# Optimization experiments

Measured on AMD Instinct MI355X. Metric: run time of the kernel, lower is better.

## Reference

```python
import jax, jax.numpy as jnp
import numpy as np
from jax.scipy.special import logsumexp

B, T, H, L = 64, 512, 768, 9


def setup_inputs() -> dict:
    key = jax.random.key(0)
    ks = jax.random.split(key, 8)
    length = jax.random.randint(ks[0], (B,), 0, T, dtype=jnp.int32)
    word2vec = jax.random.normal(ks[1], (B, T, H), dtype=jnp.float32)
    mask = jnp.ones((B, T), dtype=jnp.int32)
    label = jax.random.randint(ks[2], (B, T), 0, L, dtype=jnp.int32)
    # Linear(768 -> num_labels) params (PyTorch default init scale)
    bound = 1.0 / np.sqrt(H)
    W = jax.random.uniform(ks[3], (L, H), jnp.float32, -bound, bound)
    b = jax.random.uniform(ks[4], (L,), jnp.float32, -bound, bound)
    # CRF params (torchcrf init: uniform(-0.1, 0.1))
    start_transitions = jax.random.uniform(ks[5], (L,), jnp.float32, -0.1, 0.1)
    end_transitions = jax.random.uniform(ks[6], (L,), jnp.float32, -0.1, 0.1)
    transitions = jax.random.uniform(ks[7], (L, L), jnp.float32, -0.1, 0.1)
    return {"length": length, "word2vec": word2vec, "mask": mask, "label": label,
            "W": W, "b": b, "start_transitions": start_transitions,
            "end_transitions": end_transitions, "transitions": transitions}


def _crf_nll(emissions, tags, mask, start_transitions, end_transitions, transitions):
    # emissions [B,T,L], tags [B,T] int, mask [B,T] {0,1}
    Bn, Tn, Ln = emissions.shape
    maskf = mask.astype(emissions.dtype)
    # ---- numerator: score of the given tag sequence ----
    batch = jnp.arange(Bn)
    score = start_transitions[tags[:, 0]] + emissions[batch, 0, tags[:, 0]]
    # transition scores for steps 1..T-1, vectorized over time
    trans_sc = transitions[tags[:, :-1], tags[:, 1:]]                    # [B,T-1]
    emit_sc = jnp.take_along_axis(emissions, tags[..., None], axis=2)[..., 0]  # [B,T]
    score = score + jnp.sum((trans_sc + emit_sc[:, 1:]) * maskf[:, 1:], axis=1)
    seq_ends = jnp.sum(mask, axis=1).astype(jnp.int32) - 1
    last_tags = tags[batch, seq_ends]
    numerator = score + end_transitions[last_tags]
    # ---- denominator: log partition via forward algorithm (scan over time) ----
    em_t = jnp.transpose(emissions, (1, 0, 2))   # [T,B,L]
    mk_t = jnp.transpose(mask, (1, 0)) != 0      # [T,B]
    alpha0 = start_transitions[None, :] + em_t[0]  # [B,L]

    def step(alpha, inp):
        em_i, m_i = inp
        # alpha[b, i] + transitions[i, j] + emissions[b, j]
        nxt = logsumexp(alpha[:, :, None] + transitions[None, :, :] + em_i[:, None, :], axis=1)
        alpha = jnp.where(m_i[:, None], nxt, alpha)
        return alpha, None

    alpha, _ = jax.lax.scan(step, alpha0, (em_t[1:], mk_t[1:]))
    denominator = logsumexp(alpha + end_transitions[None, :], axis=1)
    llh = numerator - denominator
    return -jnp.mean(llh)


def reference(length, word2vec, mask, label, W, b, start_transitions, end_transitions, transitions):
    # dropout p=0.0 -> identity; Linear projection to emissions
    emissions = jnp.einsum('bth,lh->btl', word2vec, W) + b  # [B,T,L]
    return _crf_nll(emissions, label, mask, start_transitions, end_transitions, transitions)
```

## Files before the change

### kernel.cpp

```cpp
#include <hip/hip_runtime.h>
#include <hip/hip_bf16.h>


#define Bn 64
#define Tn 512
#define Hn 768
#define Ln 9
#define EMS 12
#define CS 16
#define NCHO 4
#define OT 64
#define KSTEPS 24

typedef short bf16x8 __attribute__((ext_vector_type(8)));
typedef float f32x4  __attribute__((ext_vector_type(4)));

__device__ __forceinline__ short f2bf(float f) {
    return (short)__builtin_bit_cast(unsigned short, __float2bfloat16(f));
}

#define GLOAD16(gp, lp)                                                        \
    __builtin_amdgcn_global_load_lds(                                          \
        (const __attribute__((address_space(1))) void*)(gp),                   \
        (__attribute__((address_space(3))) void*)(lp), 16, 0, 0)

__device__ __forceinline__ void pair_combine(
    const float (*MA)[Ln], const float* lgA,
    const float (*MB)[Ln], const float* lgB,
    int r, float* outM, float* outLg)
{
    float mB = lgB[0];
#pragma unroll
    for (int k = 1; k < 9; ++k) mB = fmaxf(mB, lgB[k]);
    float tA[9];
#pragma unroll
    for (int k = 0; k < 9; ++k) tA[k] = MA[r][k] * __expf(lgB[k] - mB);
    float v[9];
#pragma unroll
    for (int jj = 0; jj < 9; ++jj) {
        float acc = tA[0] * MB[0][jj];
#pragma unroll
        for (int k = 1; k < 9; ++k) acc += tA[k] * MB[k][jj];
        v[jj] = acc;
    }
    float mx = v[0];
#pragma unroll
    for (int jj = 1; jj < 9; ++jj) mx = fmaxf(mx, v[jj]);
    float inv = 1.f / mx;
#pragma unroll
    for (int jj = 0; jj < 9; ++jj) outM[jj] = v[jj] * inv;
    *outLg = lgA[r] + mB + __logf(mx);
}

__global__ __launch_bounds__(256) void emis_o_kernel(
    const float* __restrict__ wv, const float* __restrict__ Wm,
    const float* __restrict__ bias, const int* __restrict__ mask,
    const int* __restrict__ label, const float* __restrict__ trans,
    const float* __restrict__ startT,
    float* __restrict__ Mq, float* __restrict__ lgq,
    float* __restrict__ numq, int* __restrict__ msq,
    float* __restrict__ em0, int* __restrict__ cnt)
{
    __shared__ bf16x8 wlds[KSTEPS * 64];
    __shared__ __align__(16) float bufA[4][3][512];
    __shared__ float ldsE[OT][EMS];
    __shared__ int   ldsM[OT];
    __shared__ float eTs[81];
    __shared__ float sM[NCHO][Ln][Ln];
    __shared__ float sLg[NCHO][Ln];
    __shared__ float s2M[2][Ln][Ln];
    __shared__ float s2Lg[2][Ln];

    const int tid   = threadIdx.x;
    const int lane  = tid & 63;
    const int wid   = tid >> 6;
    const int bid   = blockIdx.x;
    const int b     = bid >> 3;
    const int o     = bid & 7;
    const int tbase = o * OT;

    if (bid == 0 && tid == 0) cnt[0] = 0;
    if (tid < 81) eTs[tid] = __expf(trans[tid]);

    for (int idx = tid; idx < KSTEPS * 64; idx += 256) {
        const int kk = idx >> 6, ln = idx & 63;
        const int n = ln & 15, kb2 = ln >> 4;
        bf16x8 v;
        if (n < Ln) {
            const float* src = Wm + n * Hn + kk * 32 + kb2 * 8;
#pragma unroll
            for (int j = 0; j < 8; ++j) v[j] = f2bf(src[j]);
        } else {
#pragma unroll
            for (int j = 0; j < 8; ++j) v[j] = 0;
        }
        wlds[idx] = v;
    }
    __syncthreads();

    {
        const int rowbase = bid * OT + wid * 16;
        const int rr   = lane >> 3;
        const int colf = (((lane & 7) * 16) ^ (rr << 4)) >> 2;
        const float* g0 = wv + (size_t)(rowbase + rr) * Hn + colf;
        const float* g1 = g0 + 8 * Hn;
        float* lb = &bufA[wid][0][0];

        const int m  = lane & 15;
        const int kb = lane >> 4;
        const int ph0 = m * 32 + (((kb * 32)      ^ ((m & 7) << 4)) >> 2);
        const int ph1 = m * 32 + (((kb * 32 + 16) ^ ((m & 7) << 4)) >> 2);

        f32x4 acc = {0.f, 0.f, 0.f, 0.f};

        GLOAD16(g0,      lb);        GLOAD16(g1,      lb + 256);
        GLOAD16(g0 + 32, lb + 512);  GLOAD16(g1 + 32, lb + 768);

#define EMIS_STEP(KK, SLOT)                                                    \
        {                                                                      \
            const float* s_ = lb + (SLOT) * 512;                               \
            float4 x0 = *reinterpret_cast<const float4*>(s_ + ph0);            \
            float4 x1 = *reinterpret_cast<const float4*>(s_ + ph1);            \
            bf16x8 a;                                                          \
            a[0] = f2bf(x0.x); a[1] = f2bf(x0.y);                              \
            a[2] = f2bf(x0.z); a[3] = f2bf(x0.w);                              \
            a[4] = f2bf(x1.x); a[5] = f2bf(x1.y);                              \
            a[6] = f2bf(x1.z); a[7] = f2bf(x1.w);                              \
            bf16x8 bfr = wlds[(KK) * 64 + lane];                               \
            acc = __builtin_amdgcn_mfma_f32_16x16x32_bf16(a, bfr, acc, 0, 0, 0); \
        }

        for (int kk = 0; kk < KSTEPS - 2; ++kk) {
            const int sl2 = (kk + 2) % 3;
            GLOAD16(g0 + (kk + 2) * 32, lb + sl2 * 512);
            GLOAD16(g1 + (kk + 2) * 32, lb + sl2 * 512 + 256);
            asm volatile("s_waitcnt vmcnt(4)" ::: "memory");
            EMIS_STEP(kk, kk % 3);
        }
        asm volatile("s_waitcnt vmcnt(2)" ::: "memory");
        EMIS_STEP(KSTEPS - 2, (KSTEPS - 2) % 3);
        asm volatile("s_waitcnt vmcnt(0)" ::: "memory");
        EMIS_STEP(KSTEPS - 1, (KSTEPS - 1) % 3);
#undef EMIS_STEP

        const int l = lane & 15;
        if (l < Ln) {
            const float bl = bias[l];
#pragma unroll
            for (int r = 0; r < 4; ++r) {
                const int lrow = wid * 16 + (lane >> 4) * 4 + r;
                ldsE[lrow][l] = __expf(acc[r] + bl);
            }
        }
    }
    __syncthreads();

    if (wid == 0) {
        const int gt  = tbase + lane;
        const int tag = label[b * Tn + gt];
        const int mk  = mask[b * Tn + gt];
        ldsM[lane] = mk;
        float part = 0.f; int ms = mk;
        if (gt == 0) {
            part = startT[tag] + __logf(ldsE[0][tag]);
        } else if (mk) {
            const int prev = label[b * Tn + gt - 1];
            part = trans[prev * Ln + tag] + __logf(ldsE[lane][tag]);
        }
#pragma unroll
        for (int off = 32; off > 0; off >>= 1) {
            part += __shfl_xor(part, off);
            ms   += __shfl_xor(ms, off);
        }
        if (lane == 0) { numq[bid] = part; msq[bid] = ms; }
        if (o == 0 && lane < Ln) em0[b * Ln + lane] = ldsE[0][lane];

        if (tid < NCHO * Ln) {
            float Tr[81];
#pragma unroll
            for (int i = 0; i < 81; ++i) Tr[i] = eTs[i];
            const int r = tid % Ln;
            const int c = tid / Ln;

            float v[9];
#pragma unroll
            for (int k = 0; k < 9; ++k) v[k] = (k == r) ? 1.f : 0.f;
            float lg = 0.f;

            int t0 = tbase + c * CS; if (t0 == 0) t0 = 1;
            const int t1 = tbase + (c + 1) * CS;

            int lt = t0 - tbase;
            float4 e0v = *reinterpret_cast<const float4*>(&ldsE[lt][0]);
            float4 e1v = *reinterpret_cast<const float4*>(&ldsE[lt][4]);
            float  e8  = ldsE[lt][8];
            int    mk2 = ldsM[lt];

            for (int t = t0; t < t1; ++t) {
                float4 p0 = make_float4(0.f, 0.f, 0.f, 0.f), p1 = p0;
                float  p8 = 0.f; int pm = 0;
                if (t + 1 < t1) {
                    const int nlt = t + 1 - tbase;
                    p0 = *reinterpret_cast<const float4*>(&ldsE[nlt][0]);
                    p1 = *reinterpret_cast<const float4*>(&ldsE[nlt][4]);
                    p8 = ldsE[nlt][8];
                    pm = ldsM[nlt];
                }
                if (mk2) {
                    float e[9] = {e0v.x, e0v.y, e0v.z, e0v.w,
                                  e1v.x, e1v.y, e1v.z, e1v.w, e8};
                    float nv[9];
#pragma unroll
                    for (int jj = 0; jj < 9; ++jj) {
                        float acc = v[0] * Tr[jj];
#pragma unroll
                        for (int k = 1; k < 9; ++k) acc += v[k] * Tr[k * 9 + jj];
                        nv[jj] = acc * e[jj];
                    }
                    float mx = nv[0];
#pragma unroll
                    for (int jj = 1; jj < 9; ++jj) mx = fmaxf(mx, nv[jj]);
                    float inv = 1.f / mx;
#pragma unroll
                    for (int jj = 0; jj < 9; ++jj) v[jj] = nv[jj] * inv;
                    lg += __logf(mx);
                }
                e0v = p0; e1v = p1; e8 = p8; mk2 = pm;
            }
#pragma unroll
            for (int jj = 0; jj < 9; ++jj) sM[c][r][jj] = v[jj];
            sLg[c][r] = lg;
        }

        if (tid < 2 * Ln) {
            const int p = tid / Ln, r = tid % Ln;
            float om[9], ol;
            pair_combine(sM[2 * p], sLg[2 * p], sM[2 * p + 1], sLg[2 * p + 1],
                         r, om, &ol);
#pragma unroll
            for (int jj = 0; jj < 9; ++jj) s2M[p][r][jj] = om[jj];
            s2Lg[p][r] = ol;
        }

        if (tid < Ln) {
            const int r = tid;
            float om[9], ol;
            pair_combine(s2M[0], s2Lg[0], s2M[1], s2Lg[1], r, om, &ol);
#pragma unroll
            for (int jj = 0; jj < 9; ++jj) Mq[bid * 81 + r * 9 + jj] = om[jj];
            lgq[bid * Ln + r] = ol;
        }
    }
}

__global__ __launch_bounds__(64) void comb_kernel(
    const float* __restrict__ Mq, const float* __restrict__ lgq,
    const float* __restrict__ numq, const int* __restrict__ msq,
    const float* __restrict__ em0, const int* __restrict__ label,
    const float* __restrict__ startT, const float* __restrict__ endT,
    float* __restrict__ partial, int* __restrict__ cnt, float* __restrict__ out)
{
    __shared__ float cO[8][Ln][Ln];
    __shared__ float cOl[8][Ln];
    __shared__ float cQ[4][Ln][Ln];
    __shared__ float cQl[4][Ln];
    __shared__ float cem[Ln];
    __shared__ float cnum[8];
    __shared__ int   cms[8];

    const int b = blockIdx.x, tid = threadIdx.x;

    for (int i = tid; i < 8 * 81; i += 64) ((float*)cO)[i]  = Mq[b * 648 + i];
    for (int i = tid; i < 8 * 9;  i += 64) ((float*)cOl)[i] = lgq[b * 72 + i];
    if (tid < Ln) cem[tid] = em0[b * Ln + tid];
    if (tid < 8) { cnum[tid] = numq[b * 8 + tid]; cms[tid] = msq[b * 8 + tid]; }
    __syncthreads();

    if (tid < 4 * Ln) {
        const int p = tid / Ln, r = tid % Ln;
        float om[9], ol;
        pair_combine(cO[2 * p], cOl[2 * p], cO[2 * p + 1], cOl[2 * p + 1],
                     r, om, &ol);
#pragma unroll
        for (int jj = 0; jj < 9; ++jj) cQ[p][r][jj] = om[jj];
        cQl[p][r] = ol;
    }
    __syncthreads();

    if (tid < 16) {
        const int lj = tid;
        const float NEG = -1e30f;
        float la = (lj < Ln) ? (startT[lj] + __logf(cem[lj])) : NEG;
        for (int c = 0; c < 4; ++c) {
            float mc[9];
#pragma unroll
            for (int rr = 0; rr < 9; ++rr) mc[rr] = (lj < Ln) ? cQ[c][rr][lj] : 0.f;
            float x = (lj < Ln) ? (la + cQl[c][lj]) : NEG;
            float mm = x;
#pragma unroll
            for (int off = 1; off < 16; off <<= 1) mm = fmaxf(mm, __shfl_xor(mm, off, 16));
            float w = __expf(x - mm);
            float sacc = 0.f;
#pragma unroll
            for (int rr = 0; rr < 9; ++rr) sacc += __shfl(w, rr, 16) * mc[rr];
            la = (lj < Ln) ? (mm + __logf(sacc)) : NEG;
        }
        float x = (lj < Ln) ? (la + endT[lj]) : NEG;
        float mm = x;
#pragma unroll
        for (int off = 1; off < 16; off <<= 1) mm = fmaxf(mm, __shfl_xor(mm, off, 16));
        float se = __expf(x - mm);
#pragma unroll
        for (int off = 1; off < 16; off <<= 1) se += __shfl_xor(se, off, 16);
        if (lj == 0) {
            float denom = mm + __logf(se);
            float numer = cnum[0] + cnum[1] + cnum[2] + cnum[3]
                        + cnum[4] + cnum[5] + cnum[6] + cnum[7];
            int   sm    = cms[0] + cms[1] + cms[2] + cms[3]
                        + cms[4] + cms[5] + cms[6] + cms[7];
            int   last  = label[b * Tn + sm - 1];
            partial[b]  = denom - (numer + endT[last]);
        }
    }

    int old = 0;
    if (tid == 0) {
        __threadfence();
        old = atomicAdd(cnt, 1);
    }
    old = __shfl(old, 0);
    if (old == Bn - 1) {
        __threadfence();
        float pv = partial[tid];
#pragma unroll
        for (int off = 32; off > 0; off >>= 1) pv += __shfl_xor(pv, off);
        if (tid == 0) out[0] = pv * (1.0f / Bn);
    }
}

extern "C" void kernel_launch(void* const* d_in, const int* in_sizes, int n_in,
                              void* d_out, int out_size, void* d_ws, size_t ws_size,
                              hipStream_t stream)
{
    const float* wv    = (const float*)d_in[1];
    const int*   mask  = (const int*)d_in[2];
    const int*   label = (const int*)d_in[3];
    const float* Wm    = (const float*)d_in[4];
    const float* bias  = (const float*)d_in[5];
    const float* st    = (const float*)d_in[6];
    const float* en    = (const float*)d_in[7];
    const float* tr    = (const float*)d_in[8];

    float* ws      = (float*)d_ws;
    float* Mq      = ws;
    float* lgq     = ws + 41472;
    float* numq    = ws + 46080;
    int*   msq     = (int*)(ws + 46592);
    float* em0     = ws + 47104;
    float* partial = ws + 47680;
    int*   cnt     = (int*)(ws + 47744);
    float* out     = (float*)d_out;

    hipLaunchKernelGGL(emis_o_kernel, dim3(512), dim3(256), 0, stream,
                       wv, Wm, bias, mask, label, tr, st,
                       Mq, lgq, numq, msq, em0, cnt);
    hipLaunchKernelGGL(comb_kernel, dim3(Bn), dim3(64), 0, stream,
                       Mq, lgq, numq, msq, em0, label, st, en,
                       partial, cnt, out);
}
```

Baseline: 42.21 us.

## Replace MFMA emission GEMM with fp32 register dot products and per-wave scans

The bf16 MFMA projection is removed, along with its global_load_lds triple-buffered staging and the weight staging in LDS. In its place each lane keeps its slice of W in registers, does fp32 FMAs over direct float4 loads of word2vec, and reduces each row across the wave with shuffles. The numerator and CRF chunk scans are also spread across all four waves, each handling its own 16 rows, instead of running in wave 0 only, which removes one block-wide barrier. The cost is many cross-lane shuffles per row, heavy register use for W, and only shallow memory prefetching from the unroll-by-2 loop, in exchange for exact fp32 emissions.

Result: slower. 53.08 us (+25.8%).

```diff
diff --git a/kernel.cpp b/kernel.cpp
--- a/kernel.cpp
+++ b/kernel.cpp
@@ -1,5 +1,4 @@
 #include <hip/hip_runtime.h>
-#include <hip/hip_bf16.h>
 
 
 #define Bn 64
@@ -7,22 +6,8 @@
 #define Hn 768
 #define Ln 9
 #define EMS 12
-#define CS 16
+#define OT 64
 #define NCHO 4
-#define OT 64
-#define KSTEPS 24
-
-typedef short bf16x8 __attribute__((ext_vector_type(8)));
-typedef float f32x4  __attribute__((ext_vector_type(4)));
-
-__device__ __forceinline__ short f2bf(float f) {
-    return (short)__builtin_bit_cast(unsigned short, __float2bfloat16(f));
-}
-
-#define GLOAD16(gp, lp)                                                        \
-    __builtin_amdgcn_global_load_lds(                                          \
-        (const __attribute__((address_space(1))) void*)(gp),                   \
-        (__attribute__((address_space(3))) void*)(lp), 16, 0, 0)
 
 __device__ __forceinline__ void pair_combine(
     const float (*MA)[Ln], const float* lgA,
@@ -61,15 +46,14 @@
     float* __restrict__ numq, int* __restrict__ msq,
     float* __restrict__ em0, int* __restrict__ cnt)
 {
-    __shared__ bf16x8 wlds[KSTEPS * 64];
-    __shared__ __align__(16) float bufA[4][3][512];
-    __shared__ float ldsE[OT][EMS];
+    __shared__ __align__(16) float ldsE[OT][EMS];
     __shared__ int   ldsM[OT];
-    __shared__ float eTs[81];
     __shared__ float sM[NCHO][Ln][Ln];
     __shared__ float sLg[NCHO][Ln];
     __shared__ float s2M[2][Ln][Ln];
     __shared__ float s2Lg[2][Ln];
+    __shared__ float sp[4];
+    __shared__ int   si[4];
 
     const int tid   = threadIdx.x;
     const int lane  = tid & 63;
@@ -80,160 +64,115 @@
     const int tbase = o * OT;
 
     if (bid == 0 && tid == 0) cnt[0] = 0;
-    if (tid < 81) eTs[tid] = __expf(trans[tid]);
-
-    for (int idx = tid; idx < KSTEPS * 64; idx += 256) {
-        const int kk = idx >> 6, ln = idx & 63;
-        const int n = ln & 15, kb2 = ln >> 4;
-        bf16x8 v;
-        if (n < Ln) {
-            const float* src = Wm + n * Hn + kk * 32 + kb2 * 8;
-#pragma unroll
-            for (int j = 0; j < 8; ++j) v[j] = f2bf(src[j]);
-        } else {
-#pragma unroll
-            for (int j = 0; j < 8; ++j) v[j] = 0;
-        }
-        wlds[idx] = v;
-    }
-    __syncthreads();
+
+    float4 wreg[3][9];
+#pragma unroll
+    for (int r = 0; r < 3; ++r)
+#pragma unroll
+        for (int l = 0; l < 9; ++l)
+            wreg[r][l] = *reinterpret_cast<const float4*>(
+                Wm + l * Hn + r * 256 + (lane << 2));
+
+    const float biasv = (lane < Ln) ? bias[lane] : 0.f;
+
+    const float* rowp = wv + (size_t)(bid * OT + wid * 16) * Hn + (lane << 2);
+
+#pragma unroll 2
+    for (int row = 0; row < 16; ++row) {
+        const float* src = rowp + row * Hn;
+        float4 x0 = *reinterpret_cast<const float4*>(src);
+        float4 x1 = *reinterpret_cast<const float4*>(src + 256);
+        float4 x2 = *reinterpret_cast<const float4*>(src + 512);
+        float acc[9];
+#pragma unroll
+        for (int l = 0; l < 9; ++l) {
+            float a = x0.x * wreg[0][l].x;
+            a += x0.y * wreg[0][l].y; a += x0.z * wreg[0][l].z; a += x0.w * wreg[0][l].w;
+            a += x1.x * wreg[1][l].x; a += x1.y * wreg[1][l].y;
+            a += x1.z * wreg[1][l].z; a += x1.w * wreg[1][l].w;
+            a += x2.x * wreg[2][l].x; a += x2.y * wreg[2][l].y;
+            a += x2.z * wreg[2][l].z; a += x2.w * wreg[2][l].w;
+            acc[l] = a;
+        }
+#pragma unroll
+        for (int off = 32; off > 0; off >>= 1) {
+#pragma unroll
+            for (int l = 0; l < 9; ++l) acc[l] += __shfl_xor(acc[l], off);
+        }
+        float v = acc[0];
+#pragma unroll
+        for (int l = 1; l < 9; ++l) v = (lane == l) ? acc[l] : v;
+        if (lane < Ln) ldsE[wid * 16 + row][lane] = __expf(v + biasv);
+    }
 
     {
-        const int rowbase = bid * OT + wid * 16;
-        const int rr   = lane >> 3;
-        const int colf = (((lane & 7) * 16) ^ (rr << 4)) >> 2;
-        const float* g0 = wv + (size_t)(rowbase + rr) * Hn + colf;
-        const float* g1 = g0 + 8 * Hn;
-        float* lb = &bufA[wid][0][0];
-
-        const int m  = lane & 15;
-        const int kb = lane >> 4;
-        const int ph0 = m * 32 + (((kb * 32)      ^ ((m & 7) << 4)) >> 2);
-        const int ph1 = m * 32 + (((kb * 32 + 16) ^ ((m & 7) << 4)) >> 2);
-
-        f32x4 acc = {0.f, 0.f, 0.f, 0.f};
-
-        GLOAD16(g0,      lb);        GLOAD16(g1,      lb + 256);
-        GLOAD16(g0 + 32, lb + 512);  GLOAD16(g1 + 32, lb + 768);
-
-#define EMIS_STEP(KK, SLOT)                                                    \
-        {                                                                      \
-            const float* s_ = lb + (SLOT) * 512;                               \
-            float4 x0 = *reinterpret_cast<const float4*>(s_ + ph0);            \
-            float4 x1 = *reinterpret_cast<const float4*>(s_ + ph1);            \
-            bf16x8 a;                                                          \
-            a[0] = f2bf(x0.x); a[1] = f2bf(x0.y);                              \
-            a[2] = f2bf(x0.z); a[3] = f2bf(x0.w);                              \
-            a[4] = f2bf(x1.x); a[5] = f2bf(x1.y);                              \
-            a[6] = f2bf(x1.z); a[7] = f2bf(x1.w);                              \
-            bf16x8 bfr = wlds[(KK) * 64 + lane];                               \
-            acc = __builtin_amdgcn_mfma_f32_16x16x32_bf16(a, bfr, acc, 0, 0, 0); \
-        }
-
-        for (int kk = 0; kk < KSTEPS - 2; ++kk) {
-            const int sl2 = (kk + 2) % 3;
-            GLOAD16(g0 + (kk + 2) * 32, lb + sl2 * 512);
-            GLOAD16(g1 + (kk + 2) * 32, lb + sl2 * 512 + 256);
-            asm volatile("s_waitcnt vmcnt(4)" ::: "memory");
-            EMIS_STEP(kk, kk % 3);
-        }
-        asm volatile("s_waitcnt vmcnt(2)" ::: "memory");
-        EMIS_STEP(KSTEPS - 2, (KSTEPS - 2) % 3);
-        asm volatile("s_waitcnt vmcnt(0)" ::: "memory");
-        EMIS_STEP(KSTEPS - 1, (KSTEPS - 1) % 3);
-#undef EMIS_STEP
-
-        const int l = lane & 15;
-        if (l < Ln) {
-            const float bl = bias[l];
-#pragma unroll
-            for (int r = 0; r < 4; ++r) {
-                const int lrow = wid * 16 + (lane >> 4) * 4 + r;
-                ldsE[lrow][l] = __expf(acc[r] + bl);
+        float part = 0.f; int ms = 0;
+        if (lane < 16) {
+            const int lrow = wid * 16 + lane;
+            const int gt   = tbase + lrow;
+            const int tag  = label[b * Tn + gt];
+            const int mk   = mask[b * Tn + gt];
+            ldsM[lrow] = mk; ms = mk;
+            if (gt == 0) {
+                part = startT[tag] + __logf(ldsE[0][tag]);
+            } else if (mk) {
+                const int prev = label[b * Tn + gt - 1];
+                part = trans[prev * Ln + tag] + __logf(ldsE[lrow][tag]);
             }
-        }
-    }
-    __syncthreads();
-
-    if (wid == 0) {
-        const int gt  = tbase + lane;
-        const int tag = label[b * Tn + gt];
-        const int mk  = mask[b * Tn + gt];
-        ldsM[lane] = mk;
-        float part = 0.f; int ms = mk;
-        if (gt == 0) {
-            part = startT[tag] + __logf(ldsE[0][tag]);
-        } else if (mk) {
-            const int prev = label[b * Tn + gt - 1];
-            part = trans[prev * Ln + tag] + __logf(ldsE[lane][tag]);
         }
 #pragma unroll
         for (int off = 32; off > 0; off >>= 1) {
             part += __shfl_xor(part, off);
             ms   += __shfl_xor(ms, off);
         }
-        if (lane == 0) { numq[bid] = part; msq[bid] = ms; }
+        if (lane == 0) { sp[wid] = part; si[wid] = ms; }
+    }
+
+    if (lane < Ln) {
+        float Tr[81];
+#pragma unroll
+        for (int i = 0; i < 81; ++i) Tr[i] = __expf(trans[i]);
+        const int r = lane;
+        float v[9];
+#pragma unroll
+        for (int k = 0; k < 9; ++k) v[k] = (k == r) ? 1.f : 0.f;
+        float lg = 0.f;
+        const int sstart = (tbase + wid * 16 == 0) ? 1 : 0;
+        for (int s = sstart; s < 16; ++s) {
+            const int lrow = wid * 16 + s;
+            if (ldsM[lrow]) {
+                float4 e0v = *reinterpret_cast<const float4*>(&ldsE[lrow][0]);
+                float4 e1v = *reinterpret_cast<const float4*>(&ldsE[lrow][4]);
+                float  e8  = ldsE[lrow][8];
+                float e[9] = {e0v.x, e0v.y, e0v.z, e0v.w,
+                              e1v.x, e1v.y, e1v.z, e1v.w, e8};
+                float nv[9];
+#pragma unroll
+                for (int jj = 0; jj < 9; ++jj) {
+                    float a2 = v[0] * Tr[jj];
+#pragma unroll
+                    for (int k = 1; k < 9; ++k) a2 += v[k] * Tr[k * 9 + jj];
+                    nv[jj] = a2 * e[jj];
+                }
+                float mx = nv[0];
+#pragma unroll
+                for (int jj = 1; jj < 9; ++jj) mx = fmaxf(mx, nv[jj]);
+                float inv = 1.f / mx;
+#pragma unroll
+                for (int jj = 0; jj < 9; ++jj) v[jj] = nv[jj] * inv;
+                lg += __logf(mx);
+            }
+        }
+#pragma unroll
+        for (int jj = 0; jj < 9; ++jj) sM[wid][r][jj] = v[jj];
+        sLg[wid][r] = lg;
+    }
+    __syncthreads();
+
+    if (wid == 0) {
         if (o == 0 && lane < Ln) em0[b * Ln + lane] = ldsE[0][lane];
-
-        if (tid < NCHO * Ln) {
-            float Tr[81];
-#pragma unroll
-            for (int i = 0; i < 81; ++i) Tr[i] = eTs[i];
-            const int r = tid % Ln;
-            const int c = tid / Ln;
-
-            float v[9];
-#pragma unroll
-            for (int k = 0; k < 9; ++k) v[k] = (k == r) ? 1.f : 0.f;
-            float lg = 0.f;
-
-            int t0 = tbase + c * CS; if (t0 == 0) t0 = 1;
-            const int t1 = tbase + (c + 1) * CS;
-
-            int lt = t0 - tbase;
-            float4 e0v = *reinterpret_cast<const float4*>(&ldsE[lt][0]);
-            float4 e1v = *reinterpret_cast<const float4*>(&ldsE[lt][4]);
-            float  e8  = ldsE[lt][8];
-            int    mk2 = ldsM[lt];
-
-            for (int t = t0; t < t1; ++t) {
-                float4 p0 = make_float4(0.f, 0.f, 0.f, 0.f), p1 = p0;
-                float  p8 = 0.f; int pm = 0;
-                if (t + 1 < t1) {
-                    const int nlt = t + 1 - tbase;
-                    p0 = *reinterpret_cast<const float4*>(&ldsE[nlt][0]);
-                    p1 = *reinterpret_cast<const float4*>(&ldsE[nlt][4]);
-                    p8 = ldsE[nlt][8];
-                    pm = ldsM[nlt];
-                }
-                if (mk2) {
-                    float e[9] = {e0v.x, e0v.y, e0v.z, e0v.w,
-                                  e1v.x, e1v.y, e1v.z, e1v.w, e8};
-                    float nv[9];
-#pragma unroll
-                    for (int jj = 0; jj < 9; ++jj) {
-                        float acc = v[0] * Tr[jj];
-#pragma unroll
-                        for (int k = 1; k < 9; ++k) acc += v[k] * Tr[k * 9 + jj];
-                        nv[jj] = acc * e[jj];
-                    }
-                    float mx = nv[0];
-#pragma unroll
-                    for (int jj = 1; jj < 9; ++jj) mx = fmaxf(mx, nv[jj]);
-                    float inv = 1.f / mx;
-#pragma unroll
-                    for (int jj = 0; jj < 9; ++jj) v[jj] = nv[jj] * inv;
-                    lg += __logf(mx);
-                }
-                e0v = p0; e1v = p1; e8 = p8; mk2 = pm;
-            }
-#pragma unroll
-            for (int jj = 0; jj < 9; ++jj) sM[c][r][jj] = v[jj];
-            sLg[c][r] = lg;
-        }
-
-        if (tid < 2 * Ln) {
-            const int p = tid / Ln, r = tid % Ln;
+        if (lane < 2 * Ln) {
+            const int p = lane / Ln, r = lane % Ln;
             float om[9], ol;
             pair_combine(sM[2 * p], sLg[2 * p], sM[2 * p + 1], sLg[2 * p + 1],
                          r, om, &ol);
@@ -241,14 +180,17 @@
             for (int jj = 0; jj < 9; ++jj) s2M[p][r][jj] = om[jj];
             s2Lg[p][r] = ol;
         }
-
-        if (tid < Ln) {
-            const int r = tid;
+        if (lane < Ln) {
+            const int r = lane;
             float om[9], ol;
             pair_combine(s2M[0], s2Lg[0], s2M[1], s2Lg[1], r, om, &ol);
 #pragma unroll
             for (int jj = 0; jj < 9; ++jj) Mq[bid * 81 + r * 9 + jj] = om[jj];
             lgq[bid * Ln + r] = ol;
+        }
+        if (lane == 0) {
+            numq[bid] = sp[0] + sp[1] + sp[2] + sp[3];
+            msq[bid]  = si[0] + si[1] + si[2] + si[3];
         }
     }
 }
```
